# Kernel optimization log

Hardware: AMD Instinct MI355X
Metric: run time of the kernel (lower is better)

The kernel has to match this reference:

```python
import jax, jax.numpy as jnp
import numpy as np

N = 20000      # nodes
E = 640000     # edges (avg degree 32)
K = 4          # eigenvectors (sign-invariant batch axis)
HID = 64       # hidden_dim
EDIM = 32      # edge_dim == GINE out_channels
ODIM = 64      # out_dim of rho
EPS = 0.0      # GINEConv eps (default, not learned here)


def setup_inputs() -> dict:
    key = jax.random.key(0)
    ks = jax.random.split(key, 20)
    def g(i, shape):
        return jax.random.normal(ks[i], shape, dtype=jnp.float32) / np.float32(np.sqrt(shape[0]))
    inp = {}
    inp["x"] = jax.random.normal(ks[0], (K, N, 1), dtype=jnp.float32)
    inp["edge_attr"] = jax.random.normal(ks[1], (E, EDIM), dtype=jnp.float32)
    inp["edge_index"] = jax.random.randint(ks[2], (2, E), 0, N, dtype=jnp.int32)
    in_dims = [1, HID, HID]
    out_dims = [HID, HID, EDIM]
    i = 3
    for l in range(3):
        inp[f"l{l}_We"] = g(i, (EDIM, in_dims[l])); i += 1
        inp[f"l{l}_be"] = jnp.zeros((in_dims[l],), jnp.float32)
        inp[f"l{l}_W1"] = g(i, (in_dims[l], HID)); i += 1
        inp[f"l{l}_b1"] = jnp.zeros((HID,), jnp.float32)
        inp[f"l{l}_W2"] = g(i, (HID, out_dims[l])); i += 1
        inp[f"l{l}_b2"] = jnp.zeros((out_dims[l],), jnp.float32)
    inp["Wr1"] = g(i, (EDIM, HID)); i += 1
    inp["br1"] = jnp.zeros((HID,), jnp.float32)
    inp["Wr2"] = g(i, (HID, ODIM)); i += 1
    inp["br2"] = jnp.zeros((ODIM,), jnp.float32)
    return inp


def _gine_conv(h, src, dst, edge_attr, We, be, W1, b1, W2, b2):
    # h: [K, N, F_in]; edge linear maps edge features into node feature space
    e_emb = edge_attr @ We + be                      # [E, F_in]
    msg = jax.nn.relu(h[:, src, :] + e_emb)          # [K, E, F_in] gather
    agg = jax.vmap(lambda m: jax.ops.segment_sum(m, dst, num_segments=N))(msg)  # [K, N, F_in] scatter-add
    z = (1.0 + EPS) * h + agg
    return jax.nn.relu(z @ W1 + b1) @ W2 + b2        # per-layer MLP


def _phi(h, src, dst, edge_attr, layers):
    n = len(layers)
    for l, p in enumerate(layers):
        h = _gine_conv(h, src, dst, edge_attr, *p)
        if l < n - 1:
            h = jax.nn.relu(h)
    return h  # [K, N, EDIM]


def reference(x, edge_attr, edge_index,
              l0_We, l0_be, l0_W1, l0_b1, l0_W2, l0_b2,
              l1_We, l1_be, l1_W1, l1_b1, l1_W2, l1_b2,
              l2_We, l2_be, l2_W1, l2_b1, l2_W2, l2_b2,
              Wr1, br1, Wr2, br2):
    src = edge_index[0]
    dst = edge_index[1]
    layers = [
        (l0_We, l0_be, l0_W1, l0_b1, l0_W2, l0_b2),
        (l1_We, l1_be, l1_W1, l1_b1, l1_W2, l1_b2),
        (l2_We, l2_be, l2_W1, l2_b1, l2_W2, l2_b2),
    ]
    # sign invariance: phi(x) + phi(-x)
    phi_out = _phi(x, src, dst, edge_attr, layers) + _phi(-x, src, dst, edge_attr, layers)
    pooled = jnp.sum(phi_out, axis=0)                # sum over K eigenvectors -> [N, EDIM]
    return jax.nn.relu(pooled @ Wr1 + br1) @ Wr2 + br2  # rho MLP -> [N, ODIM]
```

## Files before the change

kernel.cpp:

```cpp
#include <hip/hip_runtime.h>

#define NN 20000
#define NE 640000
#define NCH 8
#define HID 64
#define EDIM 32
#define ODIM 64

typedef __attribute__((ext_vector_type(8))) short bf16x8;
typedef __attribute__((ext_vector_type(4))) float f32x4;

__device__ __forceinline__ float b2f(unsigned short u) {
    unsigned v = ((unsigned)u) << 16;
    return __builtin_bit_cast(float, v);
}
__device__ __forceinline__ unsigned short f2b(float f) {
    unsigned u = __builtin_bit_cast(unsigned, f);
    unsigned r = (u + 0x7fffu + ((u >> 16) & 1u)) >> 16;
    return (unsigned short)r;
}
__device__ __forceinline__ f32x4 mfma16(bf16x8 a, bf16x8 b, f32x4 c) {
    return __builtin_amdgcn_mfma_f32_16x16x32_bf16(a, b, c, 0, 0, 0);
}
__device__ __forceinline__ bf16x8 load_bfrag(const unsigned short* W, int ldn, int k0, int n0, int lane) {
    int g = lane >> 4, r = lane & 15;
    bf16x8 f;
#pragma unroll
    for (int j = 0; j < 8; ++j) f[j] = (short)W[(k0 + 8 * g + j) * ldn + n0 + r];
    return f;
}

__global__ __launch_bounds__(256) void k_prep(
    const float* We1, const float* We2, const float* W11, const float* W21,
    const float* W12, const float* W22, const float* W20, const float* Wr1,
    const float* Wr2, unsigned short* bw)
{
    int gid = blockIdx.x * 256 + threadIdx.x;
    const float* src; int off;
    if      (gid < 2048)  { src = We1; off = 0; }
    else if (gid < 4096)  { src = We2; off = 2048; }
    else if (gid < 8192)  { src = W11; off = 4096; }
    else if (gid < 12288) { src = W21; off = 8192; }
    else if (gid < 16384) { src = W12; off = 12288; }
    else if (gid < 18432) { src = W22; off = 16384; }
    else if (gid < 22528) { src = W20; off = 18432; }
    else if (gid < 24576) { src = Wr1; off = 22528; }
    else                  { src = Wr2; off = 24576; }
    bw[gid] = f2b(src[gid - off]);
}

__global__ __launch_bounds__(256) void k_hist(const int* __restrict__ ei, int* __restrict__ cnt)
{
    int e = blockIdx.x * 256 + threadIdx.x;
    if (e < NE) atomicAdd(&cnt[ei[NE + e]], 1);
}

__global__ __launch_bounds__(512) void k_scan(const int* __restrict__ cnt,
                                              int* __restrict__ row, int* __restrict__ cursor)
{
    __shared__ int part[512];
    int t = threadIdx.x;
    int base = t * 40;
    int s = 0;
#pragma unroll
    for (int i = 0; i < 40; ++i) { int idx = base + i; if (idx < NN) s += cnt[idx]; }
    part[t] = s;
    __syncthreads();
    int v = s;
    for (int off = 1; off < 512; off <<= 1) {
        int add = (t >= off) ? part[t - off] : 0;
        __syncthreads();
        v += add;
        part[t] = v;
        __syncthreads();
    }
    int run = v - s;
    for (int i = 0; i < 40; ++i) {
        int idx = base + i;
        if (idx < NN) { row[idx] = run; cursor[idx] = run; run += cnt[idx]; }
    }
    if (t == 511) row[NN] = NE;
}

__global__ __launch_bounds__(256) void k_scatter(const int* __restrict__ ei,
                                                 int* __restrict__ cursor,
                                                 int* __restrict__ srcp, int* __restrict__ eidp)
{
    int e = blockIdx.x * 256 + threadIdx.x;
    if (e < NE) {
        int d = ei[NE + e];
        int pos = atomicAdd(&cursor[d], 1);
        srcp[pos] = ei[e];
        eidp[pos] = e;
    }
}

__global__ __launch_bounds__(256) void k_permea(
    const float* __restrict__ ea, const int* __restrict__ eidp,
    const float* __restrict__ We0, const float* __restrict__ be0,
    unsigned short* __restrict__ eap, float* __restrict__ emb0)
{
    int p = blockIdx.x * 256 + threadIdx.x;
    if (p >= NE) return;
    int eid = eidp[p];
    const f32x4* s4 = (const f32x4*)(ea + (size_t)eid * 32);
    float e0 = be0[0];
#pragma unroll
    for (int h = 0; h < 4; ++h) {
        f32x4 a = s4[2 * h], b = s4[2 * h + 1];
        bf16x8 o;
#pragma unroll
        for (int j = 0; j < 4; ++j) {
            e0 = fmaf(a[j], We0[h * 8 + j], e0);
            e0 = fmaf(b[j], We0[h * 8 + 4 + j], e0);
            o[j] = (short)f2b(a[j]);
            o[4 + j] = (short)f2b(b[j]);
        }
        *(bf16x8*)(eap + (size_t)p * 32 + h * 8) = o;
    }
    emb0[p] = e0;
}

__global__ __launch_bounds__(256) void k_xt(const float* __restrict__ x, float* __restrict__ xt)
{
    int n = blockIdx.x * 256 + threadIdx.x;
    if (n < NN) {
        f32x4 v = {x[n], x[NN + n], x[2 * NN + n], x[3 * NN + n]};
        *(f32x4*)(xt + (size_t)n * 4) = v;
    }
}

__global__ __launch_bounds__(256) void k_l0_gather(
    const float* __restrict__ xt, const int* __restrict__ srcp,
    const int* __restrict__ row, const float* __restrict__ emb0,
    float* __restrict__ z0)
{
    int gid = blockIdx.x * 256 + threadIdx.x;
    if (gid >= NN * 4) return;
    int d = gid >> 2, k = gid & 3;
    float accp = 0.f, accm = 0.f;
    int p1 = row[d + 1];
    for (int p = row[d]; p < p1; ++p) {
        float xs = xt[(size_t)srcp[p] * 4 + k];
        float e0 = emb0[p];
        accp += fmaxf(xs + e0, 0.f);
        accm += fmaxf(e0 - xs, 0.f);
    }
    float xd = xt[(size_t)d * 4 + k];
    z0[d * 8 + k] = xd + accp;
    z0[d * 8 + k + 4] = accm - xd;
}

__global__ __launch_bounds__(256) void k_l0_mlp(
    const float* __restrict__ z0,
    const float* __restrict__ W1, const float* __restrict__ b1,
    const unsigned short* __restrict__ W2b, const float* __restrict__ b2,
    unsigned short* __restrict__ hT)
{
    constexpr int S = 72;
    __shared__ short lds[4][16 * S];
    int lane = threadIdx.x & 63, wid = threadIdx.x >> 6, g = lane >> 4, r = lane & 15;
    short* L = lds[wid];
    bf16x8 w2f[2][4];
#pragma unroll
    for (int kk = 0; kk < 2; ++kk)
#pragma unroll
        for (int t = 0; t < 4; ++t) w2f[kk][t] = load_bfrag(W2b, 64, kk * 32, t * 16, lane);
    float b2v[4];
#pragma unroll
    for (int t = 0; t < 4; ++t) b2v[t] = b2[t * 16 + r];
    float w1a[8], w1b[8], b1a[8], b1b[8];
#pragma unroll
    for (int j = 0; j < 8; ++j) {
        w1a[j] = W1[8 * g + j];      b1a[j] = b1[8 * g + j];
        w1b[j] = W1[32 + 8 * g + j]; b1b[j] = b1[32 + 8 * g + j];
    }
    int tile = blockIdx.x * 4 + wid;
    int row0 = tile * 16;
    float zv = z0[row0 + r];
    bf16x8 a0, a1;
#pragma unroll
    for (int j = 0; j < 8; ++j) {
        a0[j] = (short)f2b(fmaxf(fmaf(zv, w1a[j], b1a[j]), 0.f));
        a1[j] = (short)f2b(fmaxf(fmaf(zv, w1b[j], b1b[j]), 0.f));
    }
    f32x4 c2[4];
#pragma unroll
    for (int t = 0; t < 4; ++t) {
        f32x4 c = {0.f, 0.f, 0.f, 0.f};
        c = mfma16(a0, w2f[0][t], c);
        c = mfma16(a1, w2f[1][t], c);
        c2[t] = c;
    }
#pragma unroll
    for (int t = 0; t < 4; ++t)
#pragma unroll
        for (int i = 0; i < 4; ++i)
            L[(4 * g + i) * S + t * 16 + r] = (short)f2b(fmaxf(c2[t][i] + b2v[t], 0.f));
    asm volatile("" ::: "memory");
    int node0 = tile * 2;
#pragma unroll
    for (int half = 0; half < 2; ++half) {
        bf16x8 v;
#pragma unroll
        for (int c = 0; c < 8; ++c) v[c] = L[(half * 8 + c) * S + lane];
        *(bf16x8*)(hT + (size_t)(node0 + half) * 512 + lane * 8) = v;
    }
}

__global__ __launch_bounds__(256) void k_gather_f(
    const int* __restrict__ srcp, const int* __restrict__ row,
    const unsigned short* __restrict__ eap,
    const unsigned short* __restrict__ Web, const float* __restrict__ be,
    const unsigned short* __restrict__ hT, unsigned short* __restrict__ z)
{
    constexpr int S4 = 66;
    __shared__ float lds[4][16 * S4];
    int lane = threadIdx.x & 63, wid = threadIdx.x >> 6, g = lane >> 4, r = lane & 15;
    float* L = lds[wid];
    bf16x8 wf[4];
#pragma unroll
    for (int t = 0; t < 4; ++t) wf[t] = load_bfrag(Web, 64, 0, t * 16, lane);
    float bev[4];
#pragma unroll
    for (int t = 0; t < 4; ++t) bev[t] = be[t * 16 + r];

    int d = blockIdx.x * 4 + wid;
    int p0 = row[d], p1 = row[d + 1];
    float acc[NCH];
#pragma unroll
    for (int c = 0; c < NCH; ++c) acc[c] = 0.f;

    bf16x8 afc = {0,0,0,0,0,0,0,0};
    int svc = 0;
    if (p0 < p1) {
        int pp = p0 + r; if (pp > p1 - 1) pp = p1 - 1;
        afc = *(const bf16x8*)(eap + (size_t)pp * 32 + 8 * g);
        svc = srcp[pp];
    }

    for (int p = p0; p < p1; p += 16) {
        int ne = p1 - p; if (ne > 16) ne = 16;
        f32x4 c[4];
#pragma unroll
        for (int t = 0; t < 4; ++t) {
            f32x4 cc = {bev[t], bev[t], bev[t], bev[t]};
            c[t] = mfma16(afc, wf[t], cc);
        }
        bf16x8 afn = afc; int svn = svc;
        int pn = p + 16;
        if (pn < p1) {
            int ppn = pn + r; if (ppn > p1 - 1) ppn = p1 - 1;
            afn = *(const bf16x8*)(eap + (size_t)ppn * 32 + 8 * g);
            svn = srcp[ppn];
        }
#pragma unroll
        for (int t = 0; t < 4; ++t)
#pragma unroll
            for (int i = 0; i < 4; ++i) {
                float v = (4 * g + i < ne) ? c[t][i] : -__builtin_inff();
                L[(4 * g + i) * S4 + t * 16 + r] = v;
            }
        asm volatile("" ::: "memory");
#pragma unroll
        for (int q = 0; q < 16; ++q) {
            int src = __builtin_amdgcn_readlane(svc, q);
            float em = L[q * S4 + lane];
            uint4 hv = *(const uint4*)(hT + (size_t)src * 512 + (lane << 3));
            unsigned dw0 = hv.x, dw1 = hv.y, dw2 = hv.z, dw3 = hv.w;
            acc[0] += fmaxf(__builtin_bit_cast(float, dw0 << 16) + em, 0.f);
            acc[1] += fmaxf(__builtin_bit_cast(float, dw0 & 0xffff0000u) + em, 0.f);
            acc[2] += fmaxf(__builtin_bit_cast(float, dw1 << 16) + em, 0.f);
            acc[3] += fmaxf(__builtin_bit_cast(float, dw1 & 0xffff0000u) + em, 0.f);
            acc[4] += fmaxf(__builtin_bit_cast(float, dw2 << 16) + em, 0.f);
            acc[5] += fmaxf(__builtin_bit_cast(float, dw2 & 0xffff0000u) + em, 0.f);
            acc[6] += fmaxf(__builtin_bit_cast(float, dw3 << 16) + em, 0.f);
            acc[7] += fmaxf(__builtin_bit_cast(float, dw3 & 0xffff0000u) + em, 0.f);
        }
        asm volatile("" ::: "memory");
        afc = afn; svc = svn;
    }

    uint4 hd = *(const uint4*)(hT + (size_t)d * 512 + (lane << 3));
    unsigned hw[4] = {hd.x, hd.y, hd.z, hd.w};
    unsigned short* zd = z + (size_t)d * 8 * 64 + lane;
#pragma unroll
    for (int j = 0; j < 4; ++j) {
        float lo = __builtin_bit_cast(float, hw[j] << 16);
        float hi = __builtin_bit_cast(float, hw[j] & 0xffff0000u);
        zd[(2 * j) * 64] = f2b(lo + acc[2 * j]);
        zd[(2 * j + 1) * 64] = f2b(hi + acc[2 * j + 1]);
    }
}

template <int OUT, bool RELU2, bool TOHT>
__global__ __launch_bounds__(256) void k_mlp(
    const unsigned short* __restrict__ z,
    const unsigned short* __restrict__ W1b, const float* __restrict__ b1,
    const unsigned short* __restrict__ W2b, const float* __restrict__ b2,
    unsigned short* __restrict__ hout)
{
    constexpr int S1 = 72;
    constexpr int S2 = (OUT == 64) ? 72 : 40;
    constexpr int NT2 = OUT / 16;
    __shared__ short lds[4][16 * S1];
    int lane = threadIdx.x & 63, wid = threadIdx.x >> 6, g = lane >> 4, r = lane & 15;
    short* L = lds[wid];

    bf16x8 w1f[2][4];
#pragma unroll
    for (int kk = 0; kk < 2; ++kk)
#pragma unroll
        for (int t = 0; t < 4; ++t) w1f[kk][t] = load_bfrag(W1b, 64, kk * 32, t * 16, lane);
    bf16x8 w2f[2][NT2];
#pragma unroll
    for (int kk = 0; kk < 2; ++kk)
#pragma unroll
        for (int t = 0; t < NT2; ++t) w2f[kk][t] = load_bfrag(W2b, OUT, kk * 32, t * 16, lane);
    float b1v[4], b2v[NT2];
#pragma unroll
    for (int t = 0; t < 4; ++t) b1v[t] = b1[t * 16 + r];
#pragma unroll
    for (int t = 0; t < NT2; ++t) b2v[t] = b2[t * 16 + r];

    int tile = blockIdx.x * 4 + wid;
    int row0 = tile * 16;

    bf16x8 a0 = *(const bf16x8*)(z + (size_t)(row0 + r) * 64 + 8 * g);
    bf16x8 a1 = *(const bf16x8*)(z + (size_t)(row0 + r) * 64 + 32 + 8 * g);
    f32x4 c1[4];
#pragma unroll
    for (int t = 0; t < 4; ++t) {
        f32x4 c = {0.f, 0.f, 0.f, 0.f};
        c = mfma16(a0, w1f[0][t], c);
        c = mfma16(a1, w1f[1][t], c);
        c1[t] = c;
    }
#pragma unroll
    for (int t = 0; t < 4; ++t)
#pragma unroll
        for (int i = 0; i < 4; ++i)
            L[(4 * g + i) * S1 + t * 16 + r] = (short)f2b(fmaxf(c1[t][i] + b1v[t], 0.f));
    asm volatile("" ::: "memory");
    bf16x8 t0 = *(const bf16x8*)(L + r * S1 + 8 * g);
    bf16x8 t1 = *(const bf16x8*)(L + r * S1 + 32 + 8 * g);
    f32x4 c2[NT2];
#pragma unroll
    for (int t = 0; t < NT2; ++t) {
        f32x4 c = {0.f, 0.f, 0.f, 0.f};
        c = mfma16(t0, w2f[0][t], c);
        c = mfma16(t1, w2f[1][t], c);
        c2[t] = c;
    }
    asm volatile("" ::: "memory");
#pragma unroll
    for (int t = 0; t < NT2; ++t)
#pragma unroll
        for (int i = 0; i < 4; ++i) {
            float v = c2[t][i] + b2v[t];
            if (RELU2) v = fmaxf(v, 0.f);
            L[(4 * g + i) * S2 + t * 16 + r] = (short)f2b(v);
        }
    asm volatile("" ::: "memory");
    if (TOHT) {
        int node0 = tile * 2;
#pragma unroll
        for (int half = 0; half < 2; ++half) {
            bf16x8 v;
#pragma unroll
            for (int c = 0; c < 8; ++c) v[c] = L[(half * 8 + c) * S2 + lane];
            *(bf16x8*)(hout + (size_t)(node0 + half) * 512 + lane * 8) = v;
        }
    } else {
        bf16x8 o0 = *(const bf16x8*)(L + r * S2 + 8 * g);
        *(bf16x8*)(hout + (size_t)(row0 + r) * OUT + 8 * g) = o0;
    }
}

__global__ __launch_bounds__(256) void k_rho(
    const unsigned short* __restrict__ h2,
    const unsigned short* __restrict__ Wr1b, const float* __restrict__ br1,
    const unsigned short* __restrict__ Wr2b, const float* __restrict__ br2,
    float* __restrict__ out)
{
    constexpr int S = 72;
    __shared__ short lds[4][16 * S];
    int lane = threadIdx.x & 63, wid = threadIdx.x >> 6, g = lane >> 4, r = lane & 15;
    short* L = lds[wid];
    int tile = blockIdx.x * 4 + wid;
    if (tile * 16 >= NN) return;
    bf16x8 w1f[4], w2f[2][4];
#pragma unroll
    for (int t = 0; t < 4; ++t) w1f[t] = load_bfrag(Wr1b, 64, 0, t * 16, lane);
#pragma unroll
    for (int kk = 0; kk < 2; ++kk)
#pragma unroll
        for (int t = 0; t < 4; ++t) w2f[kk][t] = load_bfrag(Wr2b, 64, kk * 32, t * 16, lane);
    float b1v[4], b2v[4];
#pragma unroll
    for (int t = 0; t < 4; ++t) { b1v[t] = br1[t * 16 + r]; b2v[t] = br2[t * 16 + r]; }

    int n = tile * 16 + r;
    float s[8] = {0.f, 0.f, 0.f, 0.f, 0.f, 0.f, 0.f, 0.f};
#pragma unroll
    for (int c = 0; c < NCH; ++c) {
        bf16x8 hv = *(const bf16x8*)(h2 + ((size_t)n * 8 + c) * 32 + 8 * g);
#pragma unroll
        for (int j = 0; j < 8; ++j) s[j] += b2f((unsigned short)hv[j]);
    }
    bf16x8 af;
#pragma unroll
    for (int j = 0; j < 8; ++j) af[j] = (short)f2b(s[j]);
    f32x4 c1[4];
#pragma unroll
    for (int t = 0; t < 4; ++t) {
        f32x4 c = {0.f, 0.f, 0.f, 0.f};
        c1[t] = mfma16(af, w1f[t], c);
    }
#pragma unroll
    for (int t = 0; t < 4; ++t)
#pragma unroll
        for (int i = 0; i < 4; ++i)
            L[(4 * g + i) * S + t * 16 + r] = (short)f2b(fmaxf(c1[t][i] + b1v[t], 0.f));
    asm volatile("" ::: "memory");
    bf16x8 t0 = *(const bf16x8*)(L + r * S + 8 * g);
    bf16x8 t1 = *(const bf16x8*)(L + r * S + 32 + 8 * g);
    f32x4 c2[4];
#pragma unroll
    for (int t = 0; t < 4; ++t) {
        f32x4 c = {0.f, 0.f, 0.f, 0.f};
        c = mfma16(t0, w2f[0][t], c);
        c = mfma16(t1, w2f[1][t], c);
        c2[t] = c;
    }
    int nb = tile * 16;
#pragma unroll
    for (int t = 0; t < 4; ++t)
#pragma unroll
        for (int i = 0; i < 4; ++i)
            out[(size_t)(nb + 4 * g + i) * 64 + t * 16 + r] = c2[t][i] + b2v[t];
}

extern "C" void kernel_launch(void* const* d_in, const int* in_sizes, int n_in,
                              void* d_out, int out_size, void* d_ws, size_t ws_size,
                              hipStream_t stream)
{
    const float* x   = (const float*)d_in[0];
    const float* ea  = (const float*)d_in[1];
    const int*   ei  = (const int*)d_in[2];
    const float* We0 = (const float*)d_in[3];
    const float* be0 = (const float*)d_in[4];
    const float* W10 = (const float*)d_in[5];
    const float* b10 = (const float*)d_in[6];
    const float* W20 = (const float*)d_in[7];
    const float* b20 = (const float*)d_in[8];
    const float* We1 = (const float*)d_in[9];
    const float* be1 = (const float*)d_in[10];
    const float* W11 = (const float*)d_in[11];
    const float* b11 = (const float*)d_in[12];
    const float* W21 = (const float*)d_in[13];
    const float* b21 = (const float*)d_in[14];
    const float* We2 = (const float*)d_in[15];
    const float* be2 = (const float*)d_in[16];
    const float* W12 = (const float*)d_in[17];
    const float* b12 = (const float*)d_in[18];
    const float* W22 = (const float*)d_in[19];
    const float* b22 = (const float*)d_in[20];
    const float* Wr1 = (const float*)d_in[21];
    const float* br1 = (const float*)d_in[22];
    const float* Wr2 = (const float*)d_in[23];
    const float* br2 = (const float*)d_in[24];
    float* out = (float*)d_out;

    char* base = (char*)d_ws;
    unsigned short* hT   = (unsigned short*)base; base += (size_t)NN * 512 * 2;
    unsigned short* z    = (unsigned short*)base; base += (size_t)160000 * 64 * 2;
    unsigned short* h2   = (unsigned short*)base; base += (size_t)160000 * 32 * 2;
    unsigned short* eap  = (unsigned short*)base; base += (size_t)NE * 32 * 2;
    float* emb0          = (float*)base;          base += (size_t)NE * 4;
    float* z0            = (float*)base;          base += (size_t)160000 * 4;
    float* xt            = (float*)base;          base += (size_t)NN * 4 * 4;
    int* srcp            = (int*)base;            base += (size_t)NE * 4;
    int* eidp            = (int*)base;            base += (size_t)NE * 4;
    int* row             = (int*)base;            base += 80128;
    int* cnt             = (int*)base;            base += 80128;
    int* cursor          = (int*)base;            base += 80128;
    unsigned short* bw   = (unsigned short*)base;

    const unsigned short* bWe1 = bw;
    const unsigned short* bWe2 = bw + 2048;
    const unsigned short* bW11 = bw + 4096;
    const unsigned short* bW21 = bw + 8192;
    const unsigned short* bW12 = bw + 12288;
    const unsigned short* bW22 = bw + 16384;
    const unsigned short* bW20 = bw + 18432;
    const unsigned short* bWr1 = bw + 22528;
    const unsigned short* bWr2 = bw + 24576;

    k_prep<<<112, 256, 0, stream>>>(We1, We2, W11, W21, W12, W22, W20, Wr1, Wr2, bw);
    hipMemsetAsync(cnt, 0, NN * sizeof(int), stream);
    k_hist<<<NE / 256, 256, 0, stream>>>(ei, cnt);
    k_scan<<<1, 512, 0, stream>>>(cnt, row, cursor);
    k_scatter<<<NE / 256, 256, 0, stream>>>(ei, cursor, srcp, eidp);
    k_permea<<<NE / 256, 256, 0, stream>>>(ea, eidp, We0, be0, eap, emb0);
    k_xt<<<(NN + 255) / 256, 256, 0, stream>>>(x, xt);

    k_l0_gather<<<(NN * 4 + 255) / 256, 256, 0, stream>>>(xt, srcp, row, emb0, z0);
    k_l0_mlp<<<2500, 256, 0, stream>>>(z0, W10, b10, bW20, b20, hT);

    k_gather_f<<<NN / 4, 256, 0, stream>>>(srcp, row, eap, bWe1, be1, hT, z);
    k_mlp<64, true, true><<<2500, 256, 0, stream>>>(z, bW11, b11, bW21, b21, hT);

    k_gather_f<<<NN / 4, 256, 0, stream>>>(srcp, row, eap, bWe2, be2, hT, z);
    k_mlp<32, false, false><<<2500, 256, 0, stream>>>(z, bW12, b12, bW22, b22, h2);

    k_rho<<<313, 256, 0, stream>>>(h2, bWr1, br1, bWr2, br2, out);
}
```

Measured before the change: 404.9 us.

## Parallelize layer-0 gather over edges per node, single-wave gather blocks, wider scan

The layer-0 gather now assigns half a wavefront (32 lanes) per destination node. Lanes stride over its edges, each loads a float4 of all four eigenvector channels, and the partial sums are combined with xor-shuffles. This replaces the old one-thread-per-(node,k) serial loop, which had poor load balance and little memory-level parallelism. The feature gather kernel becomes one 64-thread block per node with a launch-bounds occupancy hint, which lets the scheduler balance irregular degrees per wave. Its 16-edge inner loop is split into two unrolled halves. The CSR scan uses 1024 threads instead of 512, adding one more scan step in exchange for shorter serial per-thread loops.

```diff
diff --git a/kernel.cpp b/kernel.cpp
--- a/kernel.cpp
+++ b/kernel.cpp
@@ -55,19 +55,19 @@
     if (e < NE) atomicAdd(&cnt[ei[NE + e]], 1);
 }
 
-__global__ __launch_bounds__(512) void k_scan(const int* __restrict__ cnt,
-                                              int* __restrict__ row, int* __restrict__ cursor)
-{
-    __shared__ int part[512];
+__global__ __launch_bounds__(1024) void k_scan(const int* __restrict__ cnt,
+                                               int* __restrict__ row, int* __restrict__ cursor)
+{
+    __shared__ int part[1024];
     int t = threadIdx.x;
-    int base = t * 40;
+    int base = t * 20;
     int s = 0;
 #pragma unroll
-    for (int i = 0; i < 40; ++i) { int idx = base + i; if (idx < NN) s += cnt[idx]; }
+    for (int i = 0; i < 20; ++i) { int idx = base + i; if (idx < NN) s += cnt[idx]; }
     part[t] = s;
     __syncthreads();
     int v = s;
-    for (int off = 1; off < 512; off <<= 1) {
+    for (int off = 1; off < 1024; off <<= 1) {
         int add = (t >= off) ? part[t - off] : 0;
         __syncthreads();
         v += add;
@@ -75,11 +75,11 @@
         __syncthreads();
     }
     int run = v - s;
-    for (int i = 0; i < 40; ++i) {
+    for (int i = 0; i < 20; ++i) {
         int idx = base + i;
         if (idx < NN) { row[idx] = run; cursor[idx] = run; run += cnt[idx]; }
     }
-    if (t == 511) row[NN] = NE;
+    if (t == 1023) row[NN] = NE;
 }
 
 __global__ __launch_bounds__(256) void k_scatter(const int* __restrict__ ei,
@@ -135,20 +135,36 @@
     const int* __restrict__ row, const float* __restrict__ emb0,
     float* __restrict__ z0)
 {
-    int gid = blockIdx.x * 256 + threadIdx.x;
-    if (gid >= NN * 4) return;
-    int d = gid >> 2, k = gid & 3;
-    float accp = 0.f, accm = 0.f;
-    int p1 = row[d + 1];
-    for (int p = row[d]; p < p1; ++p) {
-        float xs = xt[(size_t)srcp[p] * 4 + k];
+    int gwave = (blockIdx.x * 256 + threadIdx.x) >> 6;
+    int half = (threadIdx.x >> 5) & 1;
+    int l = threadIdx.x & 31;
+    int d = gwave * 2 + half;
+    if (d >= NN) return;
+    int p0 = row[d], p1 = row[d + 1];
+    float ap0 = 0.f, ap1 = 0.f, ap2 = 0.f, ap3 = 0.f;
+    float am0 = 0.f, am1 = 0.f, am2 = 0.f, am3 = 0.f;
+    for (int p = p0 + l; p < p1; p += 32) {
         float e0 = emb0[p];
-        accp += fmaxf(xs + e0, 0.f);
-        accm += fmaxf(e0 - xs, 0.f);
-    }
-    float xd = xt[(size_t)d * 4 + k];
-    z0[d * 8 + k] = xd + accp;
-    z0[d * 8 + k + 4] = accm - xd;
+        f32x4 xs = *(const f32x4*)(xt + (size_t)srcp[p] * 4);
+        ap0 += fmaxf(xs[0] + e0, 0.f); am0 += fmaxf(e0 - xs[0], 0.f);
+        ap1 += fmaxf(xs[1] + e0, 0.f); am1 += fmaxf(e0 - xs[1], 0.f);
+        ap2 += fmaxf(xs[2] + e0, 0.f); am2 += fmaxf(e0 - xs[2], 0.f);
+        ap3 += fmaxf(xs[3] + e0, 0.f); am3 += fmaxf(e0 - xs[3], 0.f);
+    }
+#pragma unroll
+    for (int off = 1; off < 32; off <<= 1) {
+        ap0 += __shfl_xor(ap0, off, 64); am0 += __shfl_xor(am0, off, 64);
+        ap1 += __shfl_xor(ap1, off, 64); am1 += __shfl_xor(am1, off, 64);
+        ap2 += __shfl_xor(ap2, off, 64); am2 += __shfl_xor(am2, off, 64);
+        ap3 += __shfl_xor(ap3, off, 64); am3 += __shfl_xor(am3, off, 64);
+    }
+    if (l == 0) {
+        f32x4 xd = *(const f32x4*)(xt + (size_t)d * 4);
+        f32x4 zp = {xd[0] + ap0, xd[1] + ap1, xd[2] + ap2, xd[3] + ap3};
+        f32x4 zm = {am0 - xd[0], am1 - xd[1], am2 - xd[2], am3 - xd[3]};
+        *(f32x4*)(z0 + (size_t)d * 8) = zp;
+        *(f32x4*)(z0 + (size_t)d * 8 + 4) = zm;
+    }
 }
 
 __global__ __launch_bounds__(256) void k_l0_mlp(
@@ -208,16 +224,16 @@
     }
 }
 
-__global__ __launch_bounds__(256) void k_gather_f(
+__global__ __launch_bounds__(64, 6) void k_gather_f(
     const int* __restrict__ srcp, const int* __restrict__ row,
     const unsigned short* __restrict__ eap,
     const unsigned short* __restrict__ Web, const float* __restrict__ be,
     const unsigned short* __restrict__ hT, unsigned short* __restrict__ z)
 {
     constexpr int S4 = 66;
-    __shared__ float lds[4][16 * S4];
-    int lane = threadIdx.x & 63, wid = threadIdx.x >> 6, g = lane >> 4, r = lane & 15;
-    float* L = lds[wid];
+    __shared__ float L[16 * S4];
+    int lane = threadIdx.x;
+    int g = lane >> 4, r = lane & 15;
     bf16x8 wf[4];
 #pragma unroll
     for (int t = 0; t < 4; ++t) wf[t] = load_bfrag(Web, 64, 0, t * 16, lane);
@@ -225,7 +241,7 @@
 #pragma unroll
     for (int t = 0; t < 4; ++t) bev[t] = be[t * 16 + r];
 
-    int d = blockIdx.x * 4 + wid;
+    int d = blockIdx.x;
     int p0 = row[d], p1 = row[d + 1];
     float acc[NCH];
 #pragma unroll
@@ -263,19 +279,32 @@
             }
         asm volatile("" ::: "memory");
 #pragma unroll
-        for (int q = 0; q < 16; ++q) {
+        for (int q = 0; q < 8; ++q) {
             int src = __builtin_amdgcn_readlane(svc, q);
             float em = L[q * S4 + lane];
             uint4 hv = *(const uint4*)(hT + (size_t)src * 512 + (lane << 3));
-            unsigned dw0 = hv.x, dw1 = hv.y, dw2 = hv.z, dw3 = hv.w;
-            acc[0] += fmaxf(__builtin_bit_cast(float, dw0 << 16) + em, 0.f);
-            acc[1] += fmaxf(__builtin_bit_cast(float, dw0 & 0xffff0000u) + em, 0.f);
-            acc[2] += fmaxf(__builtin_bit_cast(float, dw1 << 16) + em, 0.f);
-            acc[3] += fmaxf(__builtin_bit_cast(float, dw1 & 0xffff0000u) + em, 0.f);
-            acc[4] += fmaxf(__builtin_bit_cast(float, dw2 << 16) + em, 0.f);
-            acc[5] += fmaxf(__builtin_bit_cast(float, dw2 & 0xffff0000u) + em, 0.f);
-            acc[6] += fmaxf(__builtin_bit_cast(float, dw3 << 16) + em, 0.f);
-            acc[7] += fmaxf(__builtin_bit_cast(float, dw3 & 0xffff0000u) + em, 0.f);
+            acc[0] += fmaxf(__builtin_bit_cast(float, hv.x << 16) + em, 0.f);
+            acc[1] += fmaxf(__builtin_bit_cast(float, hv.x & 0xffff0000u) + em, 0.f);
+            acc[2] += fmaxf(__builtin_bit_cast(float, hv.y << 16) + em, 0.f);
+            acc[3] += fmaxf(__builtin_bit_cast(float, hv.y & 0xffff0000u) + em, 0.f);
+            acc[4] += fmaxf(__builtin_bit_cast(float, hv.z << 16) + em, 0.f);
+            acc[5] += fmaxf(__builtin_bit_cast(float, hv.z & 0xffff0000u) + em, 0.f);
+            acc[6] += fmaxf(__builtin_bit_cast(float, hv.w << 16) + em, 0.f);
+            acc[7] += fmaxf(__builtin_bit_cast(float, hv.w & 0xffff0000u) + em, 0.f);
+        }
+#pragma unroll
+        for (int q = 8; q < 16; ++q) {
+            int src = __builtin_amdgcn_readlane(svc, q);
+            float em = L[q * S4 + lane];
+            uint4 hv = *(const uint4*)(hT + (size_t)src * 512 + (lane << 3));
+            acc[0] += fmaxf(__builtin_bit_cast(float, hv.x << 16) + em, 0.f);
+            acc[1] += fmaxf(__builtin_bit_cast(float, hv.x & 0xffff0000u) + em, 0.f);
+            acc[2] += fmaxf(__builtin_bit_cast(float, hv.y << 16) + em, 0.f);
+            acc[3] += fmaxf(__builtin_bit_cast(float, hv.y & 0xffff0000u) + em, 0.f);
+            acc[4] += fmaxf(__builtin_bit_cast(float, hv.z << 16) + em, 0.f);
+            acc[5] += fmaxf(__builtin_bit_cast(float, hv.z & 0xffff0000u) + em, 0.f);
+            acc[6] += fmaxf(__builtin_bit_cast(float, hv.w << 16) + em, 0.f);
+            acc[7] += fmaxf(__builtin_bit_cast(float, hv.w & 0xffff0000u) + em, 0.f);
         }
         asm volatile("" ::: "memory");
         afc = afn; svc = svn;
@@ -500,18 +529,18 @@
     k_prep<<<112, 256, 0, stream>>>(We1, We2, W11, W21, W12, W22, W20, Wr1, Wr2, bw);
     hipMemsetAsync(cnt, 0, NN * sizeof(int), stream);
     k_hist<<<NE / 256, 256, 0, stream>>>(ei, cnt);
-    k_scan<<<1, 512, 0, stream>>>(cnt, row, cursor);
+    k_scan<<<1, 1024, 0, stream>>>(cnt, row, cursor);
     k_scatter<<<NE / 256, 256, 0, stream>>>(ei, cursor, srcp, eidp);
     k_permea<<<NE / 256, 256, 0, stream>>>(ea, eidp, We0, be0, eap, emb0);
     k_xt<<<(NN + 255) / 256, 256, 0, stream>>>(x, xt);
 
-    k_l0_gather<<<(NN * 4 + 255) / 256, 256, 0, stream>>>(xt, srcp, row, emb0, z0);
+    k_l0_gather<<<(NN / 2 + 3) / 4, 256, 0, stream>>>(xt, srcp, row, emb0, z0);
     k_l0_mlp<<<2500, 256, 0, stream>>>(z0, W10, b10, bW20, b20, hT);
 
-    k_gather_f<<<NN / 4, 256, 0, stream>>>(srcp, row, eap, bWe1, be1, hT, z);
+    k_gather_f<<<NN, 64, 0, stream>>>(srcp, row, eap, bWe1, be1, hT, z);
     k_mlp<64, true, true><<<2500, 256, 0, stream>>>(z, bW11, b11, bW21, b21, hT);
 
-    k_gather_f<<<NN / 4, 256, 0, stream>>>(srcp, row, eap, bWe2, be2, hT, z);
+    k_gather_f<<<NN, 64, 0, stream>>>(srcp, row, eap, bWe2, be2, hT, z);
     k_mlp<32, false, false><<<2500, 256, 0, stream>>>(z, bW12, b12, bW22, b22, h2);
 
     k_rho<<<313, 256, 0, stream>>>(h2, bWr1, br1, bWr2, br2, out);
```

Result: slower. 778.0 us (+92.2%).
